# Optimization experiments

Hardware: AMD Instinct MI355X
Metric: run time of the kernel (lower is better)

Reference implementation:

```python
import jax, jax.numpy as jnp
import numpy as np

NUM_EXPERTS = 8
TOP_K = 2

def setup_inputs() -> dict:
    key = jax.random.key(0)
    k1, k2, k3, k4 = jax.random.split(key, 4)
    B, L, D, F, E = 2, 2048, 1024, 2048, NUM_EXPERTS
    layer_input = jax.random.normal(k1, (B, L, D), dtype=jnp.float32)
    router_w = jax.random.normal(k2, (E, D), dtype=jnp.float32) * 0.02
    # input_linear.weight.transpose(2,1) in torch -> [E, D, 2F] layout here
    w1 = jax.random.normal(k3, (E, D, 2 * F), dtype=jnp.float32) * 0.02
    # output_linear.weight.transpose(2,1) -> [E, F, D]
    w2 = jax.random.normal(k4, (E, F, D), dtype=jnp.float32) * 0.02
    return {"layer_input": layer_input, "router_w": router_w, "w1": w1, "w2": w2}


def reference(layer_input, router_w, w1, w2):
    B, L, D = layer_input.shape
    E = router_w.shape[0]
    x = layer_input.reshape(-1, D)                              # [N, D]
    router_logits = x @ router_w.T                              # [N, E]
    probs = jax.nn.softmax(router_logits.astype(jnp.float32), axis=-1)
    routing_weights, selected = jax.lax.top_k(probs, TOP_K)     # [N, K]
    routing_weights = routing_weights / routing_weights.sum(-1, keepdims=True)
    routing_weights = routing_weights.astype(x.dtype)

    out = jnp.zeros_like(x)
    # Fixed small loop over experts; same math as sorted grouped-GEMM + scatter-combine.
    for e in range(E):
        gate_e = jnp.sum(jnp.where(selected == e, routing_weights, 0.0), axis=-1)  # [N]
        gh = x @ w1[e]                                          # [N, 2F]
        g, h = jnp.split(gh, 2, axis=-1)
        y = (jax.nn.silu(g) * h) @ w2[e]                        # [N, D]
        out = out + gate_e[:, None] * y
    return out.reshape(B, L, D)
```

## Files before the change

### kernel.cpp

```cpp
#include <hip/hip_runtime.h>
#include <stdint.h>

typedef unsigned short u16;
typedef __attribute__((ext_vector_type(8))) short short8;
typedef __attribute__((ext_vector_type(4))) float floatx4;

#define NTOK 4096
#define DDIM 1024
#define FDIM 2048
#define NEXP 8

__device__ __forceinline__ u16 f2bf(float f) {
    union { float f; uint32_t u; } v; v.f = f;
    uint32_t r = v.u + 0x7fff + ((v.u >> 16) & 1);
    return (u16)(r >> 16);
}
__device__ __forceinline__ uint32_t pk2(float a, float b) {
    return (uint32_t)f2bf(a) | ((uint32_t)f2bf(b) << 16);
}
__device__ __forceinline__ void gl_lds16(const u16* g, u16* l) {
    __builtin_amdgcn_global_load_lds(
        (const __attribute__((address_space(1))) uint32_t*)g,
        (__attribute__((address_space(3))) uint32_t*)l, 16, 0, 0);
}

__global__ __launch_bounds__(256)
void router_kernel(const float* __restrict__ x, const float* __restrict__ rw,
                   int* __restrict__ topk_e, float* __restrict__ topk_w,
                   u16* __restrict__ xb) {
    const int lane = threadIdx.x & 63;
    const int wv = threadIdx.x >> 6;
    const int tok = blockIdx.x * 4 + wv;
    const float* xr = x + (size_t)tok * DDIM;
    u16* xo = xb + (size_t)tok * DDIM;
    float acc[8];
#pragma unroll
    for (int e = 0; e < 8; ++e) acc[e] = 0.f;
#pragma unroll
    for (int it = 0; it < 4; ++it) {
        int d0 = (it * 64 + lane) * 4;
        float4 xv = *(const float4*)(xr + d0);
        uint2 o = { pk2(xv.x, xv.y), pk2(xv.z, xv.w) };
        *(uint2*)(xo + d0) = o;
#pragma unroll
        for (int e = 0; e < 8; ++e) {
            float4 wv4 = *(const float4*)(rw + (size_t)e * DDIM + d0);
            acc[e] += xv.x * wv4.x + xv.y * wv4.y + xv.z * wv4.z + xv.w * wv4.w;
        }
    }
#pragma unroll
    for (int s = 32; s > 0; s >>= 1)
#pragma unroll
        for (int e = 0; e < 8; ++e) acc[e] += __shfl_down(acc[e], s);
    if (lane == 0) {
        int e0 = 0;
#pragma unroll
        for (int e = 1; e < 8; ++e) if (acc[e] > acc[e0]) e0 = e;
        int e1 = (e0 == 0) ? 1 : 0;
#pragma unroll
        for (int e = 0; e < 8; ++e) if (e != e0 && acc[e] > acc[e1]) e1 = e;
        float w0 = 1.f / (1.f + __expf(acc[e1] - acc[e0]));
        topk_e[tok * 2 + 0] = e0;
        topk_e[tok * 2 + 1] = e1;
        topk_w[tok * 2 + 0] = w0;
        topk_w[tok * 2 + 1] = 1.f - w0;
    }
}

__global__ __launch_bounds__(256)
void build_rows_all(const int* __restrict__ topk_e, int* __restrict__ counts,
                    int* __restrict__ offs, int* __restrict__ row_tok,
                    int* __restrict__ tok_row) {
    __shared__ int h[NEXP], hb[NEXP], lcnt[NEXP], loffs[NEXP];
    const int t = threadIdx.x;
    const int B = blockIdx.x;
    if (t < NEXP) { h[t] = 0; hb[t] = 0; lcnt[t] = 0; }
    __syncthreads();
    int cf[NEXP], cb[NEXP];
#pragma unroll
    for (int j = 0; j < NEXP; ++j) { cf[j] = 0; cb[j] = 0; }
    const int4* te4 = (const int4*)topk_e;
    const int gb = B * 128;
#pragma unroll
    for (int it = 0; it < 8; ++it) {
        int g = it * 256 + t;
        int4 v = te4[g];
        int before = (g < gb);
#pragma unroll
        for (int j = 0; j < NEXP; ++j) {
            int m = (v.x == j) + (v.y == j) + (v.z == j) + (v.w == j);
            cf[j] += m;
            cb[j] += before ? m : 0;
        }
    }
#pragma unroll
    for (int j = 0; j < NEXP; ++j) {
        if (cf[j]) atomicAdd(&h[j], cf[j]);
        if (cb[j]) atomicAdd(&hb[j], cb[j]);
    }
    __syncthreads();
    if (t == 0) {
        int s = 0;
        for (int e = 0; e < NEXP; ++e) { loffs[e] = s; s += h[e]; }
    }
    __syncthreads();
    const int tok = B * 256 + t;
    const int e0 = topk_e[tok * 2 + 0];
    const int e1 = topk_e[tok * 2 + 1];
    const int s0 = atomicAdd(&lcnt[e0], 1);
    const int s1 = atomicAdd(&lcnt[e1], 1);
    int r0 = loffs[e0] + hb[e0] + s0;
    row_tok[r0] = tok;
    tok_row[tok * 2 + 0] = r0;
    int r1 = loffs[e1] + hb[e1] + s1;
    row_tok[r1] = tok;
    tok_row[tok * 2 + 1] = r1;
    if (B == 0 && t < NEXP) {
        counts[t] = h[t];
        offs[t] = loffs[t];
        if (t == 0) offs[NEXP] = loffs[NEXP - 1] + h[NEXP - 1];
    }
}

__global__ __launch_bounds__(256)
void transpose_f32_bf16(const float* __restrict__ src, u16* __restrict__ dst,
                        int R, int C) {
    __shared__ float tile[64][65];
    size_t eo = (size_t)blockIdx.z * R * C;
    const float* S = src + eo;
    u16* D = dst + eo;
    int r0 = blockIdx.y * 64, c0 = blockIdx.x * 64;
    int t = threadIdx.x;
    int rr = t >> 4;
    int cc = (t & 15) * 4;
#pragma unroll
    for (int it = 0; it < 4; ++it) {
        int r = rr + it * 16;
        float4 v = *(const float4*)(S + (size_t)(r0 + r) * C + (c0 + cc));
        tile[cc + 0][r] = v.x; tile[cc + 1][r] = v.y;
        tile[cc + 2][r] = v.z; tile[cc + 3][r] = v.w;
    }
    __syncthreads();
#pragma unroll
    for (int it = 0; it < 2; ++it) {
        int u = it * 256 + t;
        int c = u >> 3;
        int rv = (u & 7) * 8;
        uint4 o;
        o.x = pk2(tile[c][rv + 0], tile[c][rv + 1]);
        o.y = pk2(tile[c][rv + 2], tile[c][rv + 3]);
        o.z = pk2(tile[c][rv + 4], tile[c][rv + 5]);
        o.w = pk2(tile[c][rv + 6], tile[c][rv + 7]);
        *(uint4*)(D + (size_t)(c0 + c) * R + (r0 + rv)) = o;
    }
}

__global__ __launch_bounds__(256, 4)
void gemm1_fast(const u16* __restrict__ xb, const u16* __restrict__ w1b,
                u16* __restrict__ act, const int* __restrict__ row_tok,
                const int* __restrict__ counts, const int* __restrict__ offs) {
    const int bid = blockIdx.x;
    const int e = bid & 7;
    const int cnt = counts[e];
    const int nmb = (cnt + 127) >> 7;
    const int j = bid >> 3;
    if (j >= nmb * 32) return;
    const int m0 = (j % nmb) * 128;
    const int n0 = (j / nmb) * 64;
    const int off = offs[e];

    __shared__ __align__(16) u16 As[2 * 128 * 32];
    __shared__ __align__(16) u16 Bs[2 * 128 * 32];

    const int t = threadIdx.x;
    const int lane = t & 63;
    const int wv = t >> 6;
    const int quad = lane >> 4;
    const int rr = lane & 15;
    const int wm = (wv & 1) * 64;
    const int wn = (wv >> 1) * 32;

    const int scol = (((lane & 3) ^ ((lane >> 3) & 3)) * 8);
    const int xq = (quad ^ ((rr >> 1) & 3)) * 8;
    const u16* arA[2];
    const u16* arB[2];
#pragma unroll
    for (int i = 0; i < 2; ++i) {
        int m = wv * 32 + i * 16 + ((lane >> 2) & 15);
        int r = m0 + m; if (r >= cnt) r = cnt - 1;
        arA[i] = xb + (size_t)row_tok[off + r] * DDIM + scol;
        size_t brow = (m < 64) ? ((size_t)e * 4096 + n0 + m)
                               : ((size_t)e * 4096 + 2048 + n0 + (m - 64));
        arB[i] = w1b + brow * DDIM + scol;
    }
    u16* dstA[2][2];
    u16* dstB[2][2];
#pragma unroll
    for (int s = 0; s < 2; ++s)
#pragma unroll
        for (int i = 0; i < 2; ++i) {
            dstA[s][i] = &As[(s * 128 + wv * 32 + i * 16) * 32];
            dstB[s][i] = &Bs[(s * 128 + wv * 32 + i * 16) * 32];
        }

    floatx4 accg[4][2] = {};
    floatx4 acch[4][2] = {};

    for (int k0 = 0; k0 < DDIM; k0 += 64) {
        __syncthreads();
#pragma unroll
        for (int s = 0; s < 2; ++s)
#pragma unroll
            for (int i = 0; i < 2; ++i) {
                gl_lds16(arA[i] + k0 + s * 32, dstA[s][i]);
                gl_lds16(arB[i] + k0 + s * 32, dstB[s][i]);
            }
        __syncthreads();

#pragma unroll
        for (int s = 0; s < 2; ++s) {
            short8 af[4], bg[2], bh[2];
#pragma unroll
            for (int mt = 0; mt < 4; ++mt)
                af[mt] = *(const short8*)&As[(s * 128 + wm + mt * 16 + rr) * 32 + xq];
#pragma unroll
            for (int nt = 0; nt < 2; ++nt) {
                bg[nt] = *(const short8*)&Bs[(s * 128 + wn + nt * 16 + rr) * 32 + xq];
                bh[nt] = *(const short8*)&Bs[(s * 128 + 64 + wn + nt * 16 + rr) * 32 + xq];
            }
#pragma unroll
            for (int mt = 0; mt < 4; ++mt)
#pragma unroll
                for (int nt = 0; nt < 2; ++nt) {
                    accg[mt][nt] = __builtin_amdgcn_mfma_f32_16x16x32_bf16(af[mt], bg[nt], accg[mt][nt], 0, 0, 0);
                    acch[mt][nt] = __builtin_amdgcn_mfma_f32_16x16x32_bf16(af[mt], bh[nt], acch[mt][nt], 0, 0, 0);
                }
        }
    }
#pragma unroll
    for (int mt = 0; mt < 4; ++mt)
#pragma unroll
        for (int nt = 0; nt < 2; ++nt)
#pragma unroll
            for (int rg = 0; rg < 4; ++rg) {
                int gm = m0 + wm + mt * 16 + quad * 4 + rg;
                if (gm < cnt) {
                    float g = accg[mt][nt][rg];
                    float h = acch[mt][nt][rg];
                    float s = g / (1.f + __expf(-g));
                    act[(size_t)(off + gm) * FDIM + (n0 + wn + nt * 16 + rr)] = f2bf(s * h);
                }
            }
}

__global__ __launch_bounds__(256, 4)
void gemm2_fast(const u16* __restrict__ act, const u16* __restrict__ w2b,
                float* __restrict__ y, const int* __restrict__ counts,
                const int* __restrict__ offs) {
    const int bid = blockIdx.x;
    const int e = bid & 7;
    const int cnt = counts[e];
    const int nmb = (cnt + 127) >> 7;
    const int j = bid >> 3;
    if (j >= nmb * 8) return;
    const int m0 = (j % nmb) * 128;
    const int n0 = (j / nmb) * 128;
    const int off = offs[e];

    __shared__ __align__(16) u16 As[2 * 128 * 32];
    __shared__ __align__(16) u16 Bs[2 * 128 * 32];

    const int t = threadIdx.x;
    const int lane = t & 63;
    const int wv = t >> 6;
    const int quad = lane >> 4;
    const int rr = lane & 15;
    const int wm = (wv & 1) * 64;
    const int wn = (wv >> 1) * 64;

    const int scol = (((lane & 3) ^ ((lane >> 3) & 3)) * 8);
    const int xq = (quad ^ ((rr >> 1) & 3)) * 8;
    const u16* arA[2];
    const u16* arB[2];
#pragma unroll
    for (int i = 0; i < 2; ++i) {
        int m = wv * 32 + i * 16 + ((lane >> 2) & 15);
        int r = m0 + m; if (r >= cnt) r = cnt - 1;
        arA[i] = act + (size_t)(off + r) * FDIM + scol;
        arB[i] = w2b + ((size_t)e * 1024 + n0 + m) * FDIM + scol;
    }
    u16* dstA[2][2];
    u16* dstB[2][2];
#pragma unroll
    for (int s = 0; s < 2; ++s)
#pragma unroll
        for (int i = 0; i < 2; ++i) {
            dstA[s][i] = &As[(s * 128 + wv * 32 + i * 16) * 32];
            dstB[s][i] = &Bs[(s * 128 + wv * 32 + i * 16) * 32];
        }

    floatx4 acc[4][4] = {};

    for (int k0 = 0; k0 < FDIM; k0 += 64) {
        __syncthreads();
#pragma unroll
        for (int s = 0; s < 2; ++s)
#pragma unroll
            for (int i = 0; i < 2; ++i) {
                gl_lds16(arA[i] + k0 + s * 32, dstA[s][i]);
                gl_lds16(arB[i] + k0 + s * 32, dstB[s][i]);
            }
        __syncthreads();

#pragma unroll
        for (int s = 0; s < 2; ++s) {
            short8 af[4], bf[4];
#pragma unroll
            for (int mt = 0; mt < 4; ++mt)
                af[mt] = *(const short8*)&As[(s * 128 + wm + mt * 16 + rr) * 32 + xq];
#pragma unroll
            for (int nt = 0; nt < 4; ++nt)
                bf[nt] = *(const short8*)&Bs[(s * 128 + wn + nt * 16 + rr) * 32 + xq];
#pragma unroll
            for (int mt = 0; mt < 4; ++mt)
#pragma unroll
                for (int nt = 0; nt < 4; ++nt)
                    acc[mt][nt] = __builtin_amdgcn_mfma_f32_16x16x32_bf16(af[mt], bf[nt], acc[mt][nt], 0, 0, 0);
        }
    }
#pragma unroll
    for (int mt = 0; mt < 4; ++mt)
#pragma unroll
        for (int rg = 0; rg < 4; ++rg) {
            int gm = m0 + wm + mt * 16 + quad * 4 + rg;
            if (gm < cnt) {
                float* yrow = y + (size_t)(off + gm) * DDIM + n0 + wn;
#pragma unroll
                for (int nt = 0; nt < 4; ++nt)
                    yrow[nt * 16 + rr] = acc[mt][nt][rg];
            }
        }
}

__global__ __launch_bounds__(256)
void combine_kernel(const float* __restrict__ y, const int* __restrict__ tok_row,
                    const float* __restrict__ topk_w, float* __restrict__ out) {
    const int tok = blockIdx.x;
    const int t = threadIdx.x;
    const int r0 = tok_row[tok * 2 + 0];
    const int r1 = tok_row[tok * 2 + 1];
    const float w0 = topk_w[tok * 2 + 0];
    const float w1 = topk_w[tok * 2 + 1];
    float4 a = *(const float4*)(y + (size_t)r0 * DDIM + t * 4);
    float4 b = *(const float4*)(y + (size_t)r1 * DDIM + t * 4);
    float4 o = { w0 * a.x + w1 * b.x, w0 * a.y + w1 * b.y,
                 w0 * a.z + w1 * b.z, w0 * a.w + w1 * b.w };
    *(float4*)(out + (size_t)tok * DDIM + t * 4) = o;
}

extern "C" void kernel_launch(void* const* d_in, const int* in_sizes, int n_in,
                              void* d_out, int out_size, void* d_ws, size_t ws_size,
                              hipStream_t stream) {
    const float* x  = (const float*)d_in[0];
    const float* rw = (const float*)d_in[1];
    const float* w1 = (const float*)d_in[2];
    const float* w2 = (const float*)d_in[3];
    float* out = (float*)d_out;

    char* ws = (char*)d_ws;
    const size_t MB = 1ull << 20;
    int*   counts   = (int*)(ws);
    int*   offs     = (int*)(ws + 128);
    int*   topk_e   = (int*)(ws + 2048);
    float* topk_w   = (float*)(ws + 2048 + 32768);
    int*   row_tok  = (int*)(ws + 2048 + 65536);
    int*   tok_row  = (int*)(ws + 2048 + 98304);
    u16*   act      = (u16*)(ws + 1 * MB);
    u16*   xb       = (u16*)(ws + 33 * MB);
    u16*   w1b      = (u16*)(ws + 41 * MB);
    u16*   w2b      = (u16*)(ws + 41 * MB);
    float* yb       = (float*)(ws + 73 * MB);

    router_kernel<<<dim3(NTOK / 4), 256, 0, stream>>>(x, rw, topk_e, topk_w, xb);
    build_rows_all<<<dim3(NTOK / 256), 256, 0, stream>>>(topk_e, counts, offs, row_tok, tok_row);
    transpose_f32_bf16<<<dim3(4096 / 64, 1024 / 64, NEXP), 256, 0, stream>>>(w1, w1b, 1024, 4096);
    gemm1_fast<<<dim3(8192), 256, 0, stream>>>(xb, w1b, act, row_tok, counts, offs);
    transpose_f32_bf16<<<dim3(1024 / 64, 2048 / 64, NEXP), 256, 0, stream>>>(w2, w2b, 2048, 1024);
    gemm2_fast<<<dim3(2048), 256, 0, stream>>>(act, w2b, yb, counts, offs);
    combine_kernel<<<dim3(NTOK), 256, 0, stream>>>(yb, tok_row, topk_w, out);
    (void)in_sizes; (void)n_in; (void)ws_size;
}
```

Measured before the change: 450.1 us.

## Enlarge gemm1 tiles to 256x128 with 512 threads and double-buffered LDS pipeline

The first grouped GEMM now uses 512-thread blocks computing 256x128 (gate+up) tiles instead of 128x64, which raises operand reuse per block. It also adds a two-stage LDS ping-pong: the next K-slice is loaded asynchronously while the current one is computed, with explicit waitcnt and barrier calls replacing the paired __syncthreads. Each wave now holds twice as many accumulators, and the block uses 128KB of LDS. This may limit occupancy to one block per CU and adds more tail waste when an expert's token count is not a multiple of 256.

```diff
diff --git a/kernel.cpp b/kernel.cpp
--- a/kernel.cpp
+++ b/kernel.cpp
@@ -23,6 +23,11 @@
         (const __attribute__((address_space(1))) uint32_t*)g,
         (__attribute__((address_space(3))) uint32_t*)l, 16, 0, 0);
 }
+
+#define WAITV0 asm volatile("s_waitcnt vmcnt(0)" ::: "memory")
+#define LGKM0  asm volatile("s_waitcnt lgkmcnt(0)" ::: "memory")
+#define BAR    __builtin_amdgcn_s_barrier()
+#define CFENCE asm volatile("" ::: "memory")
 
 __global__ __launch_bounds__(256)
 void router_kernel(const float* __restrict__ x, const float* __restrict__ rw,
@@ -155,29 +160,29 @@
     }
 }
 
-__global__ __launch_bounds__(256, 4)
+__global__ __launch_bounds__(512, 2)
 void gemm1_fast(const u16* __restrict__ xb, const u16* __restrict__ w1b,
                 u16* __restrict__ act, const int* __restrict__ row_tok,
                 const int* __restrict__ counts, const int* __restrict__ offs) {
     const int bid = blockIdx.x;
     const int e = bid & 7;
     const int cnt = counts[e];
-    const int nmb = (cnt + 127) >> 7;
+    const int nmb = (cnt + 255) >> 8;
     const int j = bid >> 3;
-    if (j >= nmb * 32) return;
-    const int m0 = (j % nmb) * 128;
-    const int n0 = (j / nmb) * 64;
+    if (j >= nmb * 16) return;
+    const int m0 = (j % nmb) * 256;
+    const int n0 = (j / nmb) * 128;
     const int off = offs[e];
 
-    __shared__ __align__(16) u16 As[2 * 128 * 32];
-    __shared__ __align__(16) u16 Bs[2 * 128 * 32];
+    __shared__ __align__(16) u16 As[2 * 2 * 256 * 32];
+    __shared__ __align__(16) u16 Bs[2 * 2 * 256 * 32];
 
     const int t = threadIdx.x;
     const int lane = t & 63;
     const int wv = t >> 6;
     const int quad = lane >> 4;
     const int rr = lane & 15;
-    const int wm = (wv & 1) * 64;
+    const int wm = (wv & 1) * 128;
     const int wn = (wv >> 1) * 32;
 
     const int scol = (((lane & 3) ^ ((lane >> 3) & 3)) * 8);
@@ -189,56 +194,55 @@
         int m = wv * 32 + i * 16 + ((lane >> 2) & 15);
         int r = m0 + m; if (r >= cnt) r = cnt - 1;
         arA[i] = xb + (size_t)row_tok[off + r] * DDIM + scol;
-        size_t brow = (m < 64) ? ((size_t)e * 4096 + n0 + m)
-                               : ((size_t)e * 4096 + 2048 + n0 + (m - 64));
+        size_t brow = (m < 128) ? ((size_t)e * 4096 + n0 + m)
+                                : ((size_t)e * 4096 + 2048 + n0 + (m - 128));
         arB[i] = w1b + brow * DDIM + scol;
     }
-    u16* dstA[2][2];
-    u16* dstB[2][2];
-#pragma unroll
-    for (int s = 0; s < 2; ++s)
-#pragma unroll
-        for (int i = 0; i < 2; ++i) {
-            dstA[s][i] = &As[(s * 128 + wv * 32 + i * 16) * 32];
-            dstB[s][i] = &Bs[(s * 128 + wv * 32 + i * 16) * 32];
-        }
-
-    floatx4 accg[4][2] = {};
-    floatx4 acch[4][2] = {};
-
-    for (int k0 = 0; k0 < DDIM; k0 += 64) {
-        __syncthreads();
-#pragma unroll
-        for (int s = 0; s < 2; ++s)
-#pragma unroll
-            for (int i = 0; i < 2; ++i) {
-                gl_lds16(arA[i] + k0 + s * 32, dstA[s][i]);
-                gl_lds16(arB[i] + k0 + s * 32, dstB[s][i]);
-            }
-        __syncthreads();
-
-#pragma unroll
-        for (int s = 0; s < 2; ++s) {
-            short8 af[4], bg[2], bh[2];
-#pragma unroll
-            for (int mt = 0; mt < 4; ++mt)
-                af[mt] = *(const short8*)&As[(s * 128 + wm + mt * 16 + rr) * 32 + xq];
-#pragma unroll
-            for (int nt = 0; nt < 2; ++nt) {
-                bg[nt] = *(const short8*)&Bs[(s * 128 + wn + nt * 16 + rr) * 32 + xq];
-                bh[nt] = *(const short8*)&Bs[(s * 128 + 64 + wn + nt * 16 + rr) * 32 + xq];
-            }
-#pragma unroll
-            for (int mt = 0; mt < 4; ++mt)
-#pragma unroll
-                for (int nt = 0; nt < 2; ++nt) {
-                    accg[mt][nt] = __builtin_amdgcn_mfma_f32_16x16x32_bf16(af[mt], bg[nt], accg[mt][nt], 0, 0, 0);
-                    acch[mt][nt] = __builtin_amdgcn_mfma_f32_16x16x32_bf16(af[mt], bh[nt], acch[mt][nt], 0, 0, 0);
-                }
-        }
-    }
-#pragma unroll
-    for (int mt = 0; mt < 4; ++mt)
+    u16* dA[2] = { &As[(wv * 32) * 32], &As[(wv * 32 + 16) * 32] };
+    u16* dB[2] = { &Bs[(wv * 32) * 32], &Bs[(wv * 32 + 16) * 32] };
+
+    floatx4 accg[8][2] = {};
+    floatx4 acch[8][2] = {};
+
+#define G1_STAGE(b, ko)                                                         \
+    { _Pragma("unroll") for (int s = 0; s < 2; ++s)                             \
+      _Pragma("unroll") for (int i = 0; i < 2; ++i) {                           \
+          gl_lds16(arA[i] + (ko) + s * 32, dA[i] + ((b) * 2 + s) * 8192);       \
+          gl_lds16(arB[i] + (ko) + s * 32, dB[i] + ((b) * 2 + s) * 8192);       \
+      } }
+
+#define G1_COMPUTE(b)                                                           \
+    { _Pragma("unroll") for (int s = 0; s < 2; ++s) {                           \
+        short8 af[8], bg[2], bh[2];                                             \
+        _Pragma("unroll") for (int mt = 0; mt < 8; ++mt)                        \
+            af[mt] = *(const short8*)&As[((b) * 2 + s) * 8192 + (wm + mt * 16 + rr) * 32 + xq]; \
+        _Pragma("unroll") for (int nt = 0; nt < 2; ++nt) {                      \
+            bg[nt] = *(const short8*)&Bs[((b) * 2 + s) * 8192 + (wn + nt * 16 + rr) * 32 + xq]; \
+            bh[nt] = *(const short8*)&Bs[((b) * 2 + s) * 8192 + (128 + wn + nt * 16 + rr) * 32 + xq]; } \
+        _Pragma("unroll") for (int mt = 0; mt < 8; ++mt)                        \
+        _Pragma("unroll") for (int nt = 0; nt < 2; ++nt) {                      \
+            accg[mt][nt] = __builtin_amdgcn_mfma_f32_16x16x32_bf16(af[mt], bg[nt], accg[mt][nt], 0, 0, 0); \
+            acch[mt][nt] = __builtin_amdgcn_mfma_f32_16x16x32_bf16(af[mt], bh[nt], acch[mt][nt], 0, 0, 0); } } }
+
+    G1_STAGE(0, 0);
+    WAITV0; BAR; CFENCE;
+    for (int p = 0; p < 7; ++p) {
+        G1_STAGE(1, (2 * p + 1) * 64);
+        G1_COMPUTE(0);
+        LGKM0; WAITV0; BAR; CFENCE;
+        G1_STAGE(0, (2 * p + 2) * 64);
+        G1_COMPUTE(1);
+        LGKM0; WAITV0; BAR; CFENCE;
+    }
+    G1_STAGE(1, 15 * 64);
+    G1_COMPUTE(0);
+    LGKM0; WAITV0; BAR; CFENCE;
+    G1_COMPUTE(1);
+#undef G1_STAGE
+#undef G1_COMPUTE
+
+#pragma unroll
+    for (int mt = 0; mt < 8; ++mt)
 #pragma unroll
         for (int nt = 0; nt < 2; ++nt)
 #pragma unroll
@@ -384,7 +388,7 @@
     router_kernel<<<dim3(NTOK / 4), 256, 0, stream>>>(x, rw, topk_e, topk_w, xb);
     build_rows_all<<<dim3(NTOK / 256), 256, 0, stream>>>(topk_e, counts, offs, row_tok, tok_row);
     transpose_f32_bf16<<<dim3(4096 / 64, 1024 / 64, NEXP), 256, 0, stream>>>(w1, w1b, 1024, 4096);
-    gemm1_fast<<<dim3(8192), 256, 0, stream>>>(xb, w1b, act, row_tok, counts, offs);
+    gemm1_fast<<<dim3(2048), 512, 0, stream>>>(xb, w1b, act, row_tok, counts, offs);
     transpose_f32_bf16<<<dim3(1024 / 64, 2048 / 64, NEXP), 256, 0, stream>>>(w2, w2b, 2048, 1024);
     gemm2_fast<<<dim3(2048), 256, 0, stream>>>(act, w2b, yb, counts, offs);
     combine_kernel<<<dim3(NTOK), 256, 0, stream>>>(yb, tok_row, topk_w, out);
```

New measurement: 461.2 us. +2.5%, slower.
